# Optimization experiments

Hardware: AMD Instinct MI355X
Metric: run time of the kernel (lower is better)

The kernel has to match this reference:

```python
import jax, jax.numpy as jnp
import numpy as np

B, C, H, W = 4, 256, 64, 64
N = H * W


def _conv1x1(x, w, b):
    # x: [B,C,H,W], w: [O,C], b: [O]  (1x1 conv == per-pixel linear)
    return jnp.einsum('bchw,oc->bohw', x, w) + b[None, :, None, None]


def setup_inputs() -> dict:
    key = jax.random.key(0)
    ks = jax.random.split(key, 11)
    s = 1.0 / np.sqrt(C)
    x = jax.random.normal(ks[0], (B, C, H, W), dtype=jnp.float32)
    mkw = lambda k: jax.random.normal(k, (C, C), dtype=jnp.float32) * s
    mkb = lambda k: jax.random.normal(k, (C,), dtype=jnp.float32) * 0.01
    return {
        'x': x,
        'w_teta': mkw(ks[1]), 'b_teta': mkb(ks[2]),
        'w_fi': mkw(ks[3]), 'b_fi': mkb(ks[4]),
        'w_gi': mkw(ks[5]), 'b_gi': mkb(ks[6]),
        'w_o1': mkw(ks[7]), 'b_o1': mkb(ks[8]),
        'w_o2': mkw(ks[9]), 'b_o2': mkb(ks[10]),
    }


def reference(x, w_teta, b_teta, w_fi, b_fi, w_gi, b_gi, w_o1, b_o1, w_o2, b_o2):
    b, c, h, w = x.shape
    n = h * w
    # 1x1 projections, flattened to [B,C,N]
    x1 = _conv1x1(x, w_teta, b_teta).reshape(b, c, n)
    x2 = _conv1x1(x, w_fi, b_fi).reshape(b, c, n)
    x3 = _conv1x1(x, w_gi, b_gi).reshape(b, c, n)
    # NOTE: original uses .view (memory reinterpretation), NOT transpose
    x1 = x1.reshape(b, n, c)
    x3 = x3.reshape(b, n, c)
    scores = jnp.einsum('bnc,bcm->bnm', x1, x2)      # [B,N,N]
    s_row = jax.nn.softmax(scores, axis=2)
    s_col = jax.nn.softmax(scores, axis=1)
    y1 = jnp.einsum('bnm,bmc->bnc', s_row, x3)       # [B,N,C]
    y2 = jnp.einsum('bnm,bmc->bnc', s_col, x3)
    # transpose(1,2) then view -> contiguous transpose + reshape
    y1 = jnp.swapaxes(y1, 1, 2).reshape(b, c, h, w)
    y2 = jnp.swapaxes(y2, 1, 2).reshape(b, c, h, w)
    o1 = _conv1x1(y1, w_o1, b_o1)
    o2 = _conv1x1(y2, w_o2, b_o2)
    xx = jnp.concatenate([x, x], axis=1)             # [B,2C,H,W]
    agg = jnp.concatenate([o1, o2], axis=1)
    return jax.nn.relu(xx + agg)
```

## Files before the change

### kernel.cpp

```cpp
#include <hip/hip_runtime.h>

#define BB   4
#define CC   256
#define NPIX 4096
#define AST2 40
#define YST  72

typedef __attribute__((ext_vector_type(8)))  short bf16x8;
typedef __attribute__((ext_vector_type(8)))  _Float16 f16x8;
typedef __attribute__((ext_vector_type(4)))  short short4v;
typedef __attribute__((ext_vector_type(16))) float f32x16;

__device__ __forceinline__ short f2h(float f) {
    _Float16 h = (_Float16)f;
    return __builtin_bit_cast(short, h);
}
__device__ __forceinline__ int cdrow(int r, int l5) {
    return (r & 3) + 8 * (r >> 2) + 4 * l5;
}
__device__ __forceinline__ short s_enc(float v) {
    float c = fmaxf(fminf(v, 127.9f), -127.9f);
    return (short)__float2int_rn(c * 256.0f);
}
__device__ __forceinline__ float s_dec(short v) {
    return (float)v * (1.0f / 256.0f);
}

__device__ __forceinline__ void mfma_core_f16(
    const short* __restrict__ A, const short* __restrict__ B, f32x16 acc[2][2])
{
    __shared__ short LA[128 * AST2], LB[128 * AST2];
    const int t = threadIdx.x;
    const int lane = t & 63, w = t >> 6;
    const int l31 = lane & 31, l5 = lane >> 5;
    const int nq = (w & 1) * 64, mq = (w >> 1) * 64;
    const int sr = t >> 1;
    const int sk = (t & 1) * 16;
    const size_t gs = (size_t)sr * 256 + sk;
    const int ls = sr * AST2 + sk;

    bf16x8 rA0 = *(const bf16x8*)(A + gs);
    bf16x8 rA1 = *(const bf16x8*)(A + gs + 8);
    bf16x8 rB0 = *(const bf16x8*)(B + gs);
    bf16x8 rB1 = *(const bf16x8*)(B + gs + 8);

    for (int k0 = 0; k0 < 256; k0 += 32) {
        __syncthreads();
        *(bf16x8*)&LA[ls]     = rA0;
        *(bf16x8*)&LA[ls + 8] = rA1;
        *(bf16x8*)&LB[ls]     = rB0;
        *(bf16x8*)&LB[ls + 8] = rB1;
        __syncthreads();
        if (k0 + 32 < 256) {
            size_t g = gs + k0 + 32;
            rA0 = *(const bf16x8*)(A + g);
            rA1 = *(const bf16x8*)(A + g + 8);
            rB0 = *(const bf16x8*)(B + g);
            rB1 = *(const bf16x8*)(B + g + 8);
        }
#pragma unroll
        for (int ks = 0; ks < 2; ks++) {
            f16x8 a[2], b[2];
#pragma unroll
            for (int s = 0; s < 2; s++) {
                a[s] = *(const f16x8*)&LA[(nq + s * 32 + l31) * AST2 + ks * 16 + l5 * 8];
                b[s] = *(const f16x8*)&LB[(mq + s * 32 + l31) * AST2 + ks * 16 + l5 * 8];
            }
#pragma unroll
            for (int s = 0; s < 2; s++)
#pragma unroll
                for (int u = 0; u < 2; u++)
                    acc[s][u] = __builtin_amdgcn_mfma_f32_32x32x16_f16(a[s], b[u], acc[s][u], 0, 0, 0);
        }
    }
}


__global__ __launch_bounds__(256) void pack_w5(
    const float* __restrict__ w0, const float* __restrict__ w1,
    const float* __restrict__ w2, const float* __restrict__ w3,
    const float* __restrict__ w4, short* __restrict__ wall)
{
    int which = blockIdx.y;
    const float* w = which == 0 ? w0 : which == 1 ? w1 : which == 2 ? w2
                   : which == 3 ? w3 : w4;
    int idx = blockIdx.x * 1024 + threadIdx.x * 4;
    float4 v = *(const float4*)(w + idx);
    short4v h;
    h.x = f2h(v.x); h.y = f2h(v.y); h.z = f2h(v.z); h.w = f2h(v.w);
    *(short4v*)(wall + which * 65536 + idx) = h;
}

__global__ __launch_bounds__(256) void pack_t_f16(
    const float* __restrict__ in, short* __restrict__ o16)
{
    __shared__ short T[32][36];
    const int b  = blockIdx.z;
    const int n0 = blockIdx.x * 32;
    const int c0 = blockIdx.y * 32;
    const float* src = in + (size_t)b * CC * NPIX;
    const int t = threadIdx.x;
    const int r = t >> 3, q = t & 7;
    float4 v = *(const float4*)(src + (size_t)(c0 + r) * NPIX + n0 + q * 4);
    T[q * 4 + 0][r] = f2h(v.x);
    T[q * 4 + 1][r] = f2h(v.y);
    T[q * 4 + 2][r] = f2h(v.z);
    T[q * 4 + 3][r] = f2h(v.w);
    __syncthreads();
    short4v o;
    o.x = T[r][q * 4 + 0];
    o.y = T[r][q * 4 + 1];
    o.z = T[r][q * 4 + 2];
    o.w = T[r][q * 4 + 3];
    size_t oo = (size_t)b * CC * NPIX + (size_t)(n0 + r) * 256 + c0 + q * 4;
    *(short4v*)(o16 + oo) = o;
}

__global__ __launch_bounds__(256) void tr16_cn(
    const short* __restrict__ in, short* __restrict__ outp)
{
    __shared__ short T[32][33];
    const int b  = blockIdx.z;
    const int n0 = blockIdx.x * 32;
    const int c0 = blockIdx.y * 32;
    const short* src = in + (size_t)b * CC * NPIX;
    short* dst = outp + (size_t)b * CC * NPIX;
    const int t = threadIdx.x;
    const int r = t >> 3, q = t & 7;
    short4v v = *(const short4v*)(src + (size_t)(c0 + r) * NPIX + n0 + q * 4);
    T[q * 4 + 0][r] = v.x;
    T[q * 4 + 1][r] = v.y;
    T[q * 4 + 2][r] = v.z;
    T[q * 4 + 3][r] = v.w;
    __syncthreads();
    short4v o;
    o.x = T[r][q * 4 + 0];
    o.y = T[r][q * 4 + 1];
    o.z = T[r][q * 4 + 2];
    o.w = T[r][q * 4 + 3];
    *(short4v*)(dst + (size_t)(n0 + r) * 256 + c0 + q * 4) = o;
}

__global__ __launch_bounds__(256) void packVt_bf(
    const short* __restrict__ x3f, short* __restrict__ Vt)
{
    __shared__ short T[32][33];
    const int b  = blockIdx.z;
    const int m0 = blockIdx.x * 32;
    const int c0 = blockIdx.y * 32;
    const short* in = x3f + (size_t)b * CC * NPIX;
    short* out = Vt + (size_t)b * CC * NPIX;
    const int t = threadIdx.x;
    const int r = t >> 3, q = t & 7;
    short4v v = *(const short4v*)(in + (size_t)(m0 + r) * CC + c0 + q * 4);
    T[q * 4 + 0][r] = v.x;
    T[q * 4 + 1][r] = v.y;
    T[q * 4 + 2][r] = v.z;
    T[q * 4 + 3][r] = v.w;
    __syncthreads();
    short4v o;
    o.x = T[r][q * 4 + 0];
    o.y = T[r][q * 4 + 1];
    o.z = T[r][q * 4 + 2];
    o.w = T[r][q * 4 + 3];
    *(short4v*)(out + (size_t)(c0 + r) * NPIX + m0 + q * 4) = o;
}


__global__ __launch_bounds__(256) void proj_mfma(
    const short* __restrict__ wpf, const short* __restrict__ xtf,
    const float* __restrict__ b_teta, const float* __restrict__ b_fi,
    const float* __restrict__ b_gi,
    short* __restrict__ x1f, short* __restrict__ x2f, short* __restrict__ x3f)
{
    const int z = blockIdx.z, p = z >> 2, b = z & 3;
    const int n0 = blockIdx.x * 128, c0 = blockIdx.y * 128;
    const size_t CN = (size_t)CC * NPIX;
    const short* Ah = wpf + p * 65536 + c0 * 256;
    const short* Bh = xtf + (size_t)b * CN + (size_t)n0 * 256;
    const float* bias = p == 0 ? b_teta : p == 1 ? b_fi : b_gi;
    short* dst = p == 0 ? x1f : p == 1 ? x2f : x3f;

    f32x16 acc[2][2] = {};
    mfma_core_f16(Ah, Bh, acc);

    const int t = threadIdx.x, lane = t & 63, w = t >> 6;
    const int l31 = lane & 31, l5 = lane >> 5;
    const int aq = (w & 1) * 64, bq = (w >> 1) * 64;
#pragma unroll
    for (int s = 0; s < 2; s++)
#pragma unroll
        for (int u = 0; u < 2; u++)
#pragma unroll
            for (int r = 0; r < 16; r++) {
                int c = c0 + aq + s * 32 + cdrow(r, l5);
                int n = n0 + bq + u * 32 + l31;
                float v = acc[s][u][r] + bias[c];
                size_t o = (size_t)b * CN + (size_t)c * NPIX + n;
                dst[o] = f2h(v);
            }
}

__global__ __launch_bounds__(256) void scores_mfma(
    const short* __restrict__ x1f, const short* __restrict__ x2tf,
    short* __restrict__ S16, float* __restrict__ pm, float* __restrict__ pl)
{
    const int m0 = blockIdx.x * 128, n0 = blockIdx.y * 128;
    f32x16 acc[2][2] = {};
    mfma_core_f16(x1f + (size_t)n0 * 256, x2tf + (size_t)m0 * 256, acc);

    const int t = threadIdx.x, lane = t & 63, w = t >> 6;
    const int l31 = lane & 31, l5 = lane >> 5;
    const int aq = (w & 1) * 64, bq = (w >> 1) * 64;
#pragma unroll
    for (int s = 0; s < 2; s++)
#pragma unroll
        for (int u = 0; u < 2; u++)
#pragma unroll
            for (int r = 0; r < 16; r++) {
                int n = n0 + aq + s * 32 + cdrow(r, l5);
                int m = m0 + bq + u * 32 + l31;
                S16[(size_t)n * NPIX + m] = s_enc(acc[s][u][r]);
            }

    const int member = w & 1;
#pragma unroll
    for (int u = 0; u < 2; u++) {
        float vmax = -1e30f;
#pragma unroll
        for (int s = 0; s < 2; s++)
#pragma unroll
            for (int r = 0; r < 16; r++) vmax = fmaxf(vmax, acc[s][u][r]);
        float vsum = 0.0f;
#pragma unroll
        for (int s = 0; s < 2; s++)
#pragma unroll
            for (int r = 0; r < 16; r++) vsum += __expf(acc[s][u][r] - vmax);
        float vmax2 = __shfl_xor(vmax, 32, 64);
        float vsum2 = __shfl_xor(vsum, 32, 64);
        float mc = fmaxf(vmax, vmax2);
        float sc = vsum * __expf(vmax - mc) + vsum2 * __expf(vmax2 - mc);
        if (l5 == 0) {
            size_t pidx = (size_t)(blockIdx.y * 2 + member) * NPIX + m0 + bq + u * 32 + l31;
            pm[pidx] = mc;
            pl[pidx] = sc;
        }
    }
}

__global__ __launch_bounds__(256) void out_mfma(
    const short* __restrict__ wof,
    const float* __restrict__ b_o1, const float* __restrict__ b_o2,
    const short* __restrict__ Yp,
    const float* __restrict__ x, float* __restrict__ out, int b)
{
    __shared__ short LA[128 * AST2], LB[128 * AST2];
    const size_t CN_ = (size_t)NPIX * CC;
    const int ch0 = blockIdx.y * 128;
    const int pix0 = blockIdx.x * 128;
    const int mode = ch0 < 256 ? 0 : 1;
    const short* W = wof + mode * 65536 + (size_t)(ch0 & 255) * 256;
    const short* Yq = Yp + (size_t)mode * 4 * CN_;
    const float* bias = mode == 0 ? b_o1 : b_o2;

    const int t = threadIdx.x, lane = t & 63, w = t >> 6;
    const int l31 = lane & 31, l5 = lane >> 5;
    const int nq = (w & 1) * 64, mq = (w >> 1) * 64;
    const int sr = t >> 1;
    const int sk = (t & 1) * 16;
    const size_t gsA = (size_t)sr * 256 + sk;
    const size_t gsB = (size_t)(pix0 + sr) * 256 + sk;
    const int ls = sr * AST2 + sk;

    f32x16 acc[2][2] = {};

    bf16x8 rA0 = *(const bf16x8*)(W + gsA);
    bf16x8 rA1 = *(const bf16x8*)(W + gsA + 8);
    f16x8 rB0, rB1;
    {
        f16x8 a0 = *(const f16x8*)(Yq + gsB);
        f16x8 a1 = *(const f16x8*)(Yq + CN_ + gsB);
        f16x8 a2 = *(const f16x8*)(Yq + 2 * CN_ + gsB);
        f16x8 a3 = *(const f16x8*)(Yq + 3 * CN_ + gsB);
        rB0 = (a0 + a1) + (a2 + a3);
        f16x8 c0 = *(const f16x8*)(Yq + gsB + 8);
        f16x8 c1 = *(const f16x8*)(Yq + CN_ + gsB + 8);
        f16x8 c2 = *(const f16x8*)(Yq + 2 * CN_ + gsB + 8);
        f16x8 c3 = *(const f16x8*)(Yq + 3 * CN_ + gsB + 8);
        rB1 = (c0 + c1) + (c2 + c3);
    }

    for (int k0 = 0; k0 < 256; k0 += 32) {
        __syncthreads();
        *(bf16x8*)&LA[ls]    = rA0;
        *(bf16x8*)&LA[ls + 8] = rA1;
        *(f16x8*)&LB[ls]     = rB0;
        *(f16x8*)&LB[ls + 8] = rB1;
        __syncthreads();
        if (k0 + 32 < 256) {
            size_t gA = gsA + k0 + 32;
            size_t gB = gsB + k0 + 32;
            rA0 = *(const bf16x8*)(W + gA);
            rA1 = *(const bf16x8*)(W + gA + 8);
            f16x8 a0 = *(const f16x8*)(Yq + gB);
            f16x8 a1 = *(const f16x8*)(Yq + CN_ + gB);
            f16x8 a2 = *(const f16x8*)(Yq + 2 * CN_ + gB);
            f16x8 a3 = *(const f16x8*)(Yq + 3 * CN_ + gB);
            rB0 = (a0 + a1) + (a2 + a3);
            f16x8 c0 = *(const f16x8*)(Yq + gB + 8);
            f16x8 c1 = *(const f16x8*)(Yq + CN_ + gB + 8);
            f16x8 c2 = *(const f16x8*)(Yq + 2 * CN_ + gB + 8);
            f16x8 c3 = *(const f16x8*)(Yq + 3 * CN_ + gB + 8);
            rB1 = (c0 + c1) + (c2 + c3);
        }
#pragma unroll
        for (int ks = 0; ks < 2; ks++) {
            f16x8 a[2], bb[2];
#pragma unroll
            for (int s = 0; s < 2; s++) {
                a[s]  = *(const f16x8*)&LA[(nq + s * 32 + l31) * AST2 + ks * 16 + l5 * 8];
                bb[s] = *(const f16x8*)&LB[(mq + s * 32 + l31) * AST2 + ks * 16 + l5 * 8];
            }
#pragma unroll
            for (int s = 0; s < 2; s++)
#pragma unroll
                for (int u = 0; u < 2; u++)
                    acc[s][u] = __builtin_amdgcn_mfma_f32_32x32x16_f16(a[s], bb[u], acc[s][u], 0, 0, 0);
        }
    }

    const int aq = (w & 1) * 64, bq = (w >> 1) * 64;
#pragma unroll
    for (int s = 0; s < 2; s++)
#pragma unroll
        for (int u = 0; u < 2; u++)
#pragma unroll
            for (int r = 0; r < 16; r++) {
                int ch = ch0 + aq + s * 32 + cdrow(r, l5);
                int pix = pix0 + bq + u * 32 + l31;
                int chm = ch & 255;
                float v = acc[s][u][r] + bias[chm] +
                          x[((size_t)b * CC + chm) * NPIX + pix];
                out[((size_t)b * 2 * CC + ch) * NPIX + pix] = fmaxf(v, 0.0f);
            }
}

__global__ __launch_bounds__(256) void stats16_kernel(
    const short* __restrict__ S16,
    const float* __restrict__ pm, const float* __restrict__ pl,
    float* __restrict__ cm, float* __restrict__ cli,
    float* __restrict__ rm, float* __restrict__ rli)
{
    __shared__ float sm[4][64], sl[4][64];
    __shared__ float red[4];
    const int t = threadIdx.x;
    if (blockIdx.x < 64) {
        const int cl = t & 63, ch = t >> 6;
        const int col = blockIdx.x * 64 + cl;
        float m = -1e30f, l = 0.0f;
        for (int i = ch * 16; i < ch * 16 + 16; i++) {
            float m2 = pm[(size_t)i * NPIX + col];
            float l2 = pl[(size_t)i * NPIX + col];
            float mn = fmaxf(m, m2);
            l = l * __expf(m - mn) + l2 * __expf(m2 - mn);
            m = mn;
        }
        sm[ch][cl] = m;
        sl[ch][cl] = l;
        __syncthreads();
        if (ch == 0) {
#pragma unroll
            for (int j = 1; j < 4; j++) {
                float m2 = sm[j][cl], l2 = sl[j][cl];
                float mn = fmaxf(m, m2);
                l = l * __expf(m - mn) + l2 * __expf(m2 - mn);
                m = mn;
            }
            cm[col]  = m;
            cli[col] = 1.0f / l;
        }
    } else {
        const int row = blockIdx.x - 64;
        const short* sp = S16 + (size_t)row * NPIX;
        const int w = t >> 6, lane = t & 63;
        float s4[16];
#pragma unroll
        for (int i = 0; i < 4; i++) {
            short4v v = *(const short4v*)(sp + (i * 256 + t) * 4);
            s4[i * 4 + 0] = s_dec(v.x);
            s4[i * 4 + 1] = s_dec(v.y);
            s4[i * 4 + 2] = s_dec(v.z);
            s4[i * 4 + 3] = s_dec(v.w);
        }
        float m = -1e30f;
#pragma unroll
        for (int i = 0; i < 16; i++) m = fmaxf(m, s4[i]);
        for (int off = 32; off; off >>= 1) m = fmaxf(m, __shfl_xor(m, off, 64));
        if (lane == 0) red[w] = m;
        __syncthreads();
        m = fmaxf(fmaxf(red[0], red[1]), fmaxf(red[2], red[3]));
        __syncthreads();
        float sum = 0.0f;
#pragma unroll
        for (int i = 0; i < 16; i++) sum += __expf(s4[i] - m);
        for (int off = 32; off; off >>= 1) sum += __shfl_xor(sum, off, 64);
        if (lane == 0) red[w] = sum;
        __syncthreads();
        if (t == 0) {
            rm[row]  = m;
            rli[row] = 1.0f / (red[0] + red[1] + red[2] + red[3]);
        }
    }
}

__global__ __launch_bounds__(256) void pv_kernel(
    const short* __restrict__ S16, const short* __restrict__ Vt,
    const float* __restrict__ rmv, const float* __restrict__ rliv,
    const float* __restrict__ cmv, const float* __restrict__ cliv,
    short* __restrict__ Yp)
{
    __shared__ short LA[64 * YST];
    __shared__ short LB[256 * YST];
    const int mode = blockIdx.z, kq = blockIdx.y;
    const int n0 = blockIdx.x * 64;
    const int kbase = kq * 1024;

    const int t = threadIdx.x, lane = t & 63, w = t >> 6;
    const int l31 = lane & 31, l5 = lane >> 5;
    const int nst = (w & 1) * 32, cb = (w >> 1) * 128;
    const int ar = t >> 2;
    const int ak = (t & 3) * 16;

    const float mrow = rmv[n0 + ar];
    const float lrow = rliv[n0 + ar];
    const short* sp = S16 + (size_t)(n0 + ar) * NPIX + kbase + ak;

    short4v sv[4];
    bf16x8 pb[8];
#pragma unroll
    for (int i = 0; i < 4; i++)
        sv[i] = *(const short4v*)(sp + i * 4);
#pragma unroll
    for (int i = 0; i < 4; i++) {
        const short* bp = Vt + (size_t)(i * 64 + ar) * NPIX + kbase + ak;
        pb[2 * i]     = *(const bf16x8*)bp;
        pb[2 * i + 1] = *(const bf16x8*)(bp + 8);
    }

    f32x16 acc[4] = {};
    for (int s = 0; s < 16; s++) {
        short4v ph[4];
        if (mode == 0) {
#pragma unroll
            for (int i = 0; i < 4; i++) {
                ph[i].x = f2h(__expf(s_dec(sv[i].x) - mrow) * lrow);
                ph[i].y = f2h(__expf(s_dec(sv[i].y) - mrow) * lrow);
                ph[i].z = f2h(__expf(s_dec(sv[i].z) - mrow) * lrow);
                ph[i].w = f2h(__expf(s_dec(sv[i].w) - mrow) * lrow);
            }
        } else {
            const int mg = kbase + s * 64 + ak;
#pragma unroll
            for (int i = 0; i < 4; i++) {
                float4 cm4 = *(const float4*)(cmv + mg + i * 4);
                float4 cl4 = *(const float4*)(cliv + mg + i * 4);
                ph[i].x = f2h(__expf(s_dec(sv[i].x) - cm4.x) * cl4.x);
                ph[i].y = f2h(__expf(s_dec(sv[i].y) - cm4.y) * cl4.y);
                ph[i].z = f2h(__expf(s_dec(sv[i].z) - cm4.z) * cl4.z);
                ph[i].w = f2h(__expf(s_dec(sv[i].w) - cm4.w) * cl4.w);
            }
        }
        __syncthreads();
#pragma unroll
        for (int i = 0; i < 4; i++)
            *(short4v*)&LA[ar * YST + ak + i * 4] = ph[i];
#pragma unroll
        for (int i = 0; i < 4; i++) {
            *(bf16x8*)&LB[(i * 64 + ar) * YST + ak]     = pb[2 * i];
            *(bf16x8*)&LB[(i * 64 + ar) * YST + ak + 8] = pb[2 * i + 1];
        }
        __syncthreads();
        if (s + 1 < 16) {
            const short* spn = sp + (s + 1) * 64;
#pragma unroll
            for (int i = 0; i < 4; i++)
                sv[i] = *(const short4v*)(spn + i * 4);
            int kg = kbase + (s + 1) * 64 + ak;
#pragma unroll
            for (int i = 0; i < 4; i++) {
                const short* bp = Vt + (size_t)(i * 64 + ar) * NPIX + kg;
                pb[2 * i]     = *(const bf16x8*)bp;
                pb[2 * i + 1] = *(const bf16x8*)(bp + 8);
            }
        }
#pragma unroll
        for (int kc = 0; kc < 4; kc++) {
            f16x8 af = *(const f16x8*)&LA[(nst + l31) * YST + kc * 16 + l5 * 8];
#pragma unroll
            for (int u = 0; u < 4; u++) {
                f16x8 bf = *(const f16x8*)&LB[(cb + u * 32 + l31) * YST + kc * 16 + l5 * 8];
                acc[u] = __builtin_amdgcn_mfma_f32_32x32x16_f16(af, bf, acc[u], 0, 0, 0);
            }
        }
    }

    short* Yo = Yp + (size_t)(mode * 4 + kq) * ((size_t)NPIX * CC);
#pragma unroll
    for (int u = 0; u < 4; u++)
#pragma unroll
        for (int r = 0; r < 16; r++) {
            int rr = cdrow(r, l5);
            Yo[(size_t)(n0 + nst + rr) * CC + cb + u * 32 + l31] = f2h(acc[u][r]);
        }
}

extern "C" void kernel_launch(void* const* d_in, const int* in_sizes, int n_in,
                              void* d_out, int out_size, void* d_ws, size_t ws_size,
                              hipStream_t stream)
{
    (void)in_sizes; (void)n_in; (void)out_size; (void)ws_size;
    const float* x      = (const float*)d_in[0];
    const float* w_teta = (const float*)d_in[1];
    const float* b_teta = (const float*)d_in[2];
    const float* w_fi   = (const float*)d_in[3];
    const float* b_fi   = (const float*)d_in[4];
    const float* w_gi   = (const float*)d_in[5];
    const float* b_gi   = (const float*)d_in[6];
    const float* w_o1   = (const float*)d_in[7];
    const float* b_o1   = (const float*)d_in[8];
    const float* w_o2   = (const float*)d_in[9];
    const float* b_o2   = (const float*)d_in[10];
    float* out = (float*)d_out;

    const size_t CN = (size_t)CC * NPIX;
    const size_t NN = (size_t)NPIX * NPIX;
    short* wsp   = (short*)d_ws;
    short* S16   = wsp;
    short* Yp    = S16 + NN;
    short* x1f   = Yp + 8 * CN;
    short* x2tf  = x1f + BB * CN;
    short* Vtb   = x2tf + BB * CN;
    float* cm    = (float*)(Vtb + BB * CN);
    float* cli   = cm + NPIX;
    float* rm    = cli + NPIX;
    float* rli   = rm + NPIX;
    float* pm    = rli + NPIX;
    float* pl    = pm + 64 * NPIX;
    short* wall  = (short*)(pl + 64 * NPIX);
    short* wpf   = wall;
    short* wof   = wall + 3 * 65536;
    short* xtf  = Yp;
    short* x2f  = S16;
    short* x3f  = S16 + BB * CN;

    dim3 blk(256);
    pack_w5<<<dim3(64, 5), blk, 0, stream>>>(w_teta, w_fi, w_gi, w_o1, w_o2, wall);
    pack_t_f16<<<dim3(128, 8, 4), blk, 0, stream>>>(x, xtf);

    proj_mfma<<<dim3(32, 2, 12), blk, 0, stream>>>(
        wpf, xtf, b_teta, b_fi, b_gi, x1f, x2f, x3f);

    tr16_cn<<<dim3(128, 8, 4), blk, 0, stream>>>(x2f, x2tf);
    packVt_bf<<<dim3(128, 8, 4), blk, 0, stream>>>(x3f, Vtb);

    for (int b = 0; b < BB; b++) {
        scores_mfma<<<dim3(32, 32), blk, 0, stream>>>(
            x1f + b * CN, x2tf + b * CN, S16, pm, pl);
        stats16_kernel<<<dim3(64 + NPIX), blk, 0, stream>>>(
            S16, pm, pl, cm, cli, rm, rli);
        pv_kernel<<<dim3(64, 4, 2), blk, 0, stream>>>(
            S16, Vtb + b * CN, rm, rli, cm, cli, Yp);
        out_mfma<<<dim3(32, 4), blk, 0, stream>>>(
            wof, b_o1, b_o2, Yp, x, out, b);
    }
}
```

Before: 455.8 us.

## Fuse row and column softmax PV passes into one dual-accumulator kernel

After: 489.2 us. +7.3%, slower.

```diff
diff --git a/kernel.cpp b/kernel.cpp
--- a/kernel.cpp
+++ b/kernel.cpp
@@ -260,7 +260,7 @@
     const int pix0 = blockIdx.x * 128;
     const int mode = ch0 < 256 ? 0 : 1;
     const short* W = wof + mode * 65536 + (size_t)(ch0 & 255) * 256;
-    const short* Yq = Yp + (size_t)mode * 4 * CN_;
+    const short* Yq = Yp + (size_t)mode * 8 * CN_;
     const float* bias = mode == 0 ? b_o1 : b_o2;
 
     const int t = threadIdx.x, lane = t & 63, w = t >> 6;
@@ -278,16 +278,13 @@
     bf16x8 rA1 = *(const bf16x8*)(W + gsA + 8);
     f16x8 rB0, rB1;
     {
-        f16x8 a0 = *(const f16x8*)(Yq + gsB);
-        f16x8 a1 = *(const f16x8*)(Yq + CN_ + gsB);
-        f16x8 a2 = *(const f16x8*)(Yq + 2 * CN_ + gsB);
-        f16x8 a3 = *(const f16x8*)(Yq + 3 * CN_ + gsB);
-        rB0 = (a0 + a1) + (a2 + a3);
-        f16x8 c0 = *(const f16x8*)(Yq + gsB + 8);
-        f16x8 c1 = *(const f16x8*)(Yq + CN_ + gsB + 8);
-        f16x8 c2 = *(const f16x8*)(Yq + 2 * CN_ + gsB + 8);
-        f16x8 c3 = *(const f16x8*)(Yq + 3 * CN_ + gsB + 8);
-        rB1 = (c0 + c1) + (c2 + c3);
+        rB0 = *(const f16x8*)(Yq + gsB);
+        rB1 = *(const f16x8*)(Yq + gsB + 8);
+#pragma unroll
+        for (int q = 1; q < 8; q++) {
+            rB0 = rB0 + *(const f16x8*)(Yq + (size_t)q * CN_ + gsB);
+            rB1 = rB1 + *(const f16x8*)(Yq + (size_t)q * CN_ + gsB + 8);
+        }
     }
 
     for (int k0 = 0; k0 < 256; k0 += 32) {
@@ -302,16 +299,13 @@
             size_t gB = gsB + k0 + 32;
             rA0 = *(const bf16x8*)(W + gA);
             rA1 = *(const bf16x8*)(W + gA + 8);
-            f16x8 a0 = *(const f16x8*)(Yq + gB);
-            f16x8 a1 = *(const f16x8*)(Yq + CN_ + gB);
-            f16x8 a2 = *(const f16x8*)(Yq + 2 * CN_ + gB);
-            f16x8 a3 = *(const f16x8*)(Yq + 3 * CN_ + gB);
-            rB0 = (a0 + a1) + (a2 + a3);
-            f16x8 c0 = *(const f16x8*)(Yq + gB + 8);
-            f16x8 c1 = *(const f16x8*)(Yq + CN_ + gB + 8);
-            f16x8 c2 = *(const f16x8*)(Yq + 2 * CN_ + gB + 8);
-            f16x8 c3 = *(const f16x8*)(Yq + 3 * CN_ + gB + 8);
-            rB1 = (c0 + c1) + (c2 + c3);
+            rB0 = *(const f16x8*)(Yq + gB);
+            rB1 = *(const f16x8*)(Yq + gB + 8);
+#pragma unroll
+            for (int q = 1; q < 8; q++) {
+                rB0 = rB0 + *(const f16x8*)(Yq + (size_t)q * CN_ + gB);
+                rB1 = rB1 + *(const f16x8*)(Yq + (size_t)q * CN_ + gB + 8);
+            }
         }
 #pragma unroll
         for (int ks = 0; ks < 2; ks++) {
@@ -413,17 +407,18 @@
     }
 }
 
-__global__ __launch_bounds__(256) void pv_kernel(
+__global__ __launch_bounds__(256) void pv_dual_kernel(
     const short* __restrict__ S16, const short* __restrict__ Vt,
     const float* __restrict__ rmv, const float* __restrict__ rliv,
     const float* __restrict__ cmv, const float* __restrict__ cliv,
     short* __restrict__ Yp)
 {
-    __shared__ short LA[64 * YST];
+    __shared__ short LA0[64 * YST];
+    __shared__ short LA1[64 * YST];
     __shared__ short LB[256 * YST];
-    const int mode = blockIdx.z, kq = blockIdx.y;
+    const int kq = blockIdx.y;
     const int n0 = blockIdx.x * 64;
-    const int kbase = kq * 1024;
+    const int kbase = kq * 512;
 
     const int t = threadIdx.x, lane = t & 63, w = t >> 6;
     const int l31 = lane & 31, l5 = lane >> 5;
@@ -447,40 +442,39 @@
         pb[2 * i + 1] = *(const bf16x8*)(bp + 8);
     }
 
-    f32x16 acc[4] = {};
-    for (int s = 0; s < 16; s++) {
-        short4v ph[4];
-        if (mode == 0) {
-#pragma unroll
-            for (int i = 0; i < 4; i++) {
-                ph[i].x = f2h(__expf(s_dec(sv[i].x) - mrow) * lrow);
-                ph[i].y = f2h(__expf(s_dec(sv[i].y) - mrow) * lrow);
-                ph[i].z = f2h(__expf(s_dec(sv[i].z) - mrow) * lrow);
-                ph[i].w = f2h(__expf(s_dec(sv[i].w) - mrow) * lrow);
-            }
-        } else {
-            const int mg = kbase + s * 64 + ak;
-#pragma unroll
-            for (int i = 0; i < 4; i++) {
-                float4 cm4 = *(const float4*)(cmv + mg + i * 4);
-                float4 cl4 = *(const float4*)(cliv + mg + i * 4);
-                ph[i].x = f2h(__expf(s_dec(sv[i].x) - cm4.x) * cl4.x);
-                ph[i].y = f2h(__expf(s_dec(sv[i].y) - cm4.y) * cl4.y);
-                ph[i].z = f2h(__expf(s_dec(sv[i].z) - cm4.z) * cl4.z);
-                ph[i].w = f2h(__expf(s_dec(sv[i].w) - cm4.w) * cl4.w);
-            }
-        }
-        __syncthreads();
-#pragma unroll
-        for (int i = 0; i < 4; i++)
-            *(short4v*)&LA[ar * YST + ak + i * 4] = ph[i];
+    f32x16 acc0[4] = {};
+    f32x16 acc1[4] = {};
+    for (int s = 0; s < 8; s++) {
+        short4v ph0[4], ph1[4];
+        const int mg = kbase + s * 64 + ak;
+#pragma unroll
+        for (int i = 0; i < 4; i++) {
+            float4 cm4 = *(const float4*)(cmv + mg + i * 4);
+            float4 cl4 = *(const float4*)(cliv + mg + i * 4);
+            float d0 = s_dec(sv[i].x), d1 = s_dec(sv[i].y);
+            float d2 = s_dec(sv[i].z), d3 = s_dec(sv[i].w);
+            ph0[i].x = f2h(__expf(d0 - mrow) * lrow);
+            ph0[i].y = f2h(__expf(d1 - mrow) * lrow);
+            ph0[i].z = f2h(__expf(d2 - mrow) * lrow);
+            ph0[i].w = f2h(__expf(d3 - mrow) * lrow);
+            ph1[i].x = f2h(__expf(d0 - cm4.x) * cl4.x);
+            ph1[i].y = f2h(__expf(d1 - cm4.y) * cl4.y);
+            ph1[i].z = f2h(__expf(d2 - cm4.z) * cl4.z);
+            ph1[i].w = f2h(__expf(d3 - cm4.w) * cl4.w);
+        }
+        __syncthreads();
+#pragma unroll
+        for (int i = 0; i < 4; i++) {
+            *(short4v*)&LA0[ar * YST + ak + i * 4] = ph0[i];
+            *(short4v*)&LA1[ar * YST + ak + i * 4] = ph1[i];
+        }
 #pragma unroll
         for (int i = 0; i < 4; i++) {
             *(bf16x8*)&LB[(i * 64 + ar) * YST + ak]     = pb[2 * i];
             *(bf16x8*)&LB[(i * 64 + ar) * YST + ak + 8] = pb[2 * i + 1];
         }
         __syncthreads();
-        if (s + 1 < 16) {
+        if (s + 1 < 8) {
             const short* spn = sp + (s + 1) * 64;
 #pragma unroll
             for (int i = 0; i < 4; i++)
@@ -495,22 +489,27 @@
         }
 #pragma unroll
         for (int kc = 0; kc < 4; kc++) {
-            f16x8 af = *(const f16x8*)&LA[(nst + l31) * YST + kc * 16 + l5 * 8];
+            f16x8 af0 = *(const f16x8*)&LA0[(nst + l31) * YST + kc * 16 + l5 * 8];
+            f16x8 af1 = *(const f16x8*)&LA1[(nst + l31) * YST + kc * 16 + l5 * 8];
 #pragma unroll
             for (int u = 0; u < 4; u++) {
                 f16x8 bf = *(const f16x8*)&LB[(cb + u * 32 + l31) * YST + kc * 16 + l5 * 8];
-                acc[u] = __builtin_amdgcn_mfma_f32_32x32x16_f16(af, bf, acc[u], 0, 0, 0);
-            }
-        }
-    }
-
-    short* Yo = Yp + (size_t)(mode * 4 + kq) * ((size_t)NPIX * CC);
+                acc0[u] = __builtin_amdgcn_mfma_f32_32x32x16_f16(af0, bf, acc0[u], 0, 0, 0);
+                acc1[u] = __builtin_amdgcn_mfma_f32_32x32x16_f16(af1, bf, acc1[u], 0, 0, 0);
+            }
+        }
+    }
+
+    short* Yo0 = Yp + (size_t)kq * ((size_t)NPIX * CC);
+    short* Yo1 = Yp + (size_t)(8 + kq) * ((size_t)NPIX * CC);
 #pragma unroll
     for (int u = 0; u < 4; u++)
 #pragma unroll
         for (int r = 0; r < 16; r++) {
             int rr = cdrow(r, l5);
-            Yo[(size_t)(n0 + nst + rr) * CC + cb + u * 32 + l31] = f2h(acc[u][r]);
+            size_t o = (size_t)(n0 + nst + rr) * CC + cb + u * 32 + l31;
+            Yo0[o] = f2h(acc0[u][r]);
+            Yo1[o] = f2h(acc1[u][r]);
         }
 }
 
@@ -537,7 +536,7 @@
     short* wsp   = (short*)d_ws;
     short* S16   = wsp;
     short* Yp    = S16 + NN;
-    short* x1f   = Yp + 8 * CN;
+    short* x1f   = Yp + 16 * CN;
     short* x2tf  = x1f + BB * CN;
     short* Vtb   = x2tf + BB * CN;
     float* cm    = (float*)(Vtb + BB * CN);
@@ -568,7 +567,7 @@
             x1f + b * CN, x2tf + b * CN, S16, pm, pl);
         stats16_kernel<<<dim3(64 + NPIX), blk, 0, stream>>>(
             S16, pm, pl, cm, cli, rm, rli);
-        pv_kernel<<<dim3(64, 4, 2), blk, 0, stream>>>(
+        pv_dual_kernel<<<dim3(64, 8), blk, 0, stream>>>(
             S16, Vtb + b * CN, rm, rli, cm, cli, Yp);
         out_mfma<<<dim3(32, 4), blk, 0, stream>>>(
             wof, b_o1, b_o2, Yp, x, out, b);
```
